# Optimization experiments

Measured on AMD Instinct MI355X. Metric: run time of the kernel, lower is better.

## Reference

```python
import jax, jax.numpy as jnp
import numpy as np

B, S, IN_DIM, H_DIM, OUT_DIM, N_LAYERS = 64, 1024, 256, 512, 256, 2


def setup_inputs() -> dict:
    key = jax.random.key(0)
    ks = jax.random.split(key, 16)
    scale = 0.05

    def W(k, shape):
        return (jax.random.normal(k, shape, jnp.float32) * scale)

    inp = {
        "input": jax.random.normal(ks[0], (B, S, IN_DIM), jnp.float32),
        "hidden_state": jnp.zeros((B, N_LAYERS, H_DIM), jnp.float32),
    }
    ki = 1
    for i in range(N_LAYERS):
        d_in = IN_DIM if i == 0 else H_DIM
        for g in ("z", "r", "g"):
            inp[f"W{g}_in_{i}"] = W(ks[ki], (d_in, H_DIM)); ki += 1
            inp[f"W{g}_h_{i}"] = W(ks[ki], (H_DIM, H_DIM)); ki += 1
            inp[f"b{g}_{i}"] = jnp.zeros((H_DIM,), jnp.float32)
    inp["Wo"] = W(ks[ki], (H_DIM, OUT_DIM)); ki += 1
    inp["bo"] = jnp.zeros((OUT_DIM,), jnp.float32)
    return inp


def _gru_layer(xs, h0, Wzi, Wzh, bz, Wri, Wrh, br, Wgi, Wgh, bg):
    # Precompute input projections for all timesteps (same math as per-step Linear).
    xz = jnp.einsum("bsi,ih->bsh", xs, Wzi)
    xr = jnp.einsum("bsi,ih->bsh", xs, Wri)
    xg = jnp.einsum("bsi,ih->bsh", xs, Wgi)

    def step(h, t):
        xz_t, xr_t, xg_t = t
        z = jax.nn.sigmoid(xz_t + h @ Wzh + bz)
        r = jax.nn.sigmoid(xr_t + h @ Wrh + br)
        g = jnp.tanh(xg_t + (h * r) @ Wgh + bg)
        h_new = z * h + (1.0 - z) * g
        return h_new, h_new

    h_last, hs = jax.lax.scan(
        step, h0,
        (jnp.swapaxes(xz, 0, 1), jnp.swapaxes(xr, 0, 1), jnp.swapaxes(xg, 0, 1)))
    return jnp.swapaxes(hs, 0, 1), h_last  # (B,S,H), (B,H)


def reference(input, hidden_state,
              Wz_in_0, Wz_h_0, bz_0, Wr_in_0, Wr_h_0, br_0, Wg_in_0, Wg_h_0, bg_0,
              Wz_in_1, Wz_h_1, bz_1, Wr_in_1, Wr_h_1, br_1, Wg_in_1, Wg_h_1, bg_1,
              Wo, bo):
    layers = [
        (Wz_in_0, Wz_h_0, bz_0, Wr_in_0, Wr_h_0, br_0, Wg_in_0, Wg_h_0, bg_0),
        (Wz_in_1, Wz_h_1, bz_1, Wr_in_1, Wr_h_1, br_1, Wg_in_1, Wg_h_1, bg_1),
    ]
    b = input.shape[0]
    seq = input
    finals = []
    for i, p in enumerate(layers):
        seq, h_last = _gru_layer(seq, hidden_state[:, i, :], *p)
        finals.append(h_last)
    y = jnp.einsum("bsh,ho->bso", seq, Wo) + bo
    # Faithful to original: torch.cat(layer_states) then reshape to (B, L, H)
    h_out = jnp.concatenate(finals, axis=0).reshape(b, len(layers), H_DIM)
    return y, h_out
```

## Files before the change

### kernel.cpp

```cpp
#include <hip/hip_runtime.h>
#include <stdint.h>

typedef unsigned short u16;
typedef short v8s __attribute__((ext_vector_type(8)));
typedef float v4f __attribute__((ext_vector_type(4)));

#define B_ 64
#define S_ 1024
#define IN_ 256
#define H_ 512
#define OUT_ 256
#define BS_ (B_ * S_)
#define GS_ ((size_t)BS_ * H_)
#define HP_ (H_ + 8)
#define KP1_ (1024 + 8)
#define FPAD_ 16

static __device__ __forceinline__ u16 f2bf(float f) {
  uint32_t u = __float_as_uint(f);
  u += 0x7FFFu + ((u >> 16) & 1u);
  return (u16)(u >> 16);
}
static __device__ __forceinline__ float bf2f(u16 h) {
  return __uint_as_float(((uint32_t)h) << 16);
}
static __device__ __forceinline__ v4f mfma16(v8s a, v8s b, v4f c) {
  return __builtin_amdgcn_mfma_f32_16x16x32_bf16(a, b, c, 0, 0, 0);
}
static __device__ __forceinline__ uint64_t cload64(const uint64_t* p) {
  return __hip_atomic_load(p, __ATOMIC_RELAXED, __HIP_MEMORY_SCOPE_AGENT);
}
static __device__ __forceinline__ void cstore64(uint64_t* p, uint64_t v) {
  __hip_atomic_store(p, v, __ATOMIC_RELAXED, __HIP_MEMORY_SCOPE_AGENT);
}
static __device__ __forceinline__ void cstore32(uint32_t* p, uint32_t v) {
  __hip_atomic_store(p, v, __ATOMIC_RELAXED, __HIP_MEMORY_SCOPE_AGENT);
}
static __device__ __forceinline__ void pollge(const uint32_t* p, uint32_t want) {
  while (__hip_atomic_load(p, __ATOMIC_RELAXED, __HIP_MEMORY_SCOPE_AGENT) < want)
    __builtin_amdgcn_s_sleep(1);
}
template <int NS>
static __device__ __forceinline__ void slab_barrier(uint32_t* flagbase,
                                                    int slab, uint32_t want,
                                                    int tid) {
  __syncthreads();
  if (tid == 0)
    __hip_atomic_store(flagbase + slab * FPAD_, want, __ATOMIC_RELAXED,
                       __HIP_MEMORY_SCOPE_AGENT);
  if (tid < NS) pollge(flagbase + tid * FPAD_, want);
  __syncthreads();
}

__global__ void cast_input_kernel(const float* __restrict__ src,
                                  u16* __restrict__ dst, int n4) {
  int i = blockIdx.x * blockDim.x + threadIdx.x;
  int stride = gridDim.x * blockDim.x;
  for (; i < n4; i += stride) {
    float4 v = ((const float4*)src)[i];
    uint32_t lo = (uint32_t)f2bf(v.x) | ((uint32_t)f2bf(v.y) << 16);
    uint32_t hi = (uint32_t)f2bf(v.z) | ((uint32_t)f2bf(v.w) << 16);
    ((uint2*)dst)[i] = make_uint2(lo, hi);
  }
}

__global__ void pack_transpose_k(const float* __restrict__ src,
                                 u16* __restrict__ dst, int K, int N,
                                 int dstK, int k0) {
  int i = blockIdx.x * blockDim.x + threadIdx.x;
  int total = K * N;
  int stride = gridDim.x * blockDim.x;
  for (; i < total; i += stride) {
    int n = i / K, k = i - n * K;
    dst[(size_t)n * dstK + k0 + k] = f2bf(src[(size_t)k * N + n]);
  }
}

__global__ void __launch_bounds__(256) gemm_kernel(
    const u16* __restrict__ A, const u16* __restrict__ Bt, int N, int K,
    u16* __restrict__ outb, float* __restrict__ outf,
    const float* __restrict__ bias, int mode) {
  const int bn = blockIdx.x * 64;
  const int bm = blockIdx.y * 64;
  const int w = threadIdx.x >> 6;
  const int lane = threadIdx.x & 63;
  const int wm = (w >> 1) * 32, wn = (w & 1) * 32;
  const int fr = lane & 15;
  const int kb = (lane >> 4) * 8;
  v4f acc00 = {0,0,0,0}, acc01 = {0,0,0,0}, acc10 = {0,0,0,0}, acc11 = {0,0,0,0};
  const u16* a0p = A + (size_t)(bm + wm + fr) * K + kb;
  const u16* a1p = a0p + (size_t)16 * K;
  const u16* b0p = Bt + (size_t)(bn + wn + fr) * K + kb;
  const u16* b1p = b0p + (size_t)16 * K;
  for (int kk = 0; kk < K; kk += 32) {
    v8s a0 = *(const v8s*)(a0p + kk);
    v8s a1 = *(const v8s*)(a1p + kk);
    v8s b0 = *(const v8s*)(b0p + kk);
    v8s b1 = *(const v8s*)(b1p + kk);
    acc00 = mfma16(a0, b0, acc00);
    acc01 = mfma16(a0, b1, acc01);
    acc10 = mfma16(a1, b0, acc10);
    acc11 = mfma16(a1, b1, acc11);
  }
  v4f accs[2][2] = {{acc00, acc01}, {acc10, acc11}};
  const int rb = (lane >> 4) * 4;
#pragma unroll
  for (int mi = 0; mi < 2; ++mi)
#pragma unroll
    for (int ni = 0; ni < 2; ++ni)
#pragma unroll
      for (int j = 0; j < 4; ++j) {
        int row = bm + wm + mi * 16 + rb + j;
        int col = bn + wn + ni * 16 + fr;
        float v = accs[mi][ni][j];
        if (mode == 0) {
          int gate = col >> 9, c = col & (H_ - 1);
          outb[(size_t)gate * GS_ + (size_t)row * H_ + c] = f2bf(v);
        } else {
          outf[(size_t)row * N + col] = v + bias[col];
        }
      }
}

__global__ void __launch_bounds__(256, 1) gru_pipe_kernel(
    const u16* xproj,
    const u16* __restrict__ Wht0,
    const u16* __restrict__ Wstk1,
    const float* __restrict__ bz0, const float* __restrict__ br0,
    const float* __restrict__ bg0,
    const float* __restrict__ bz1, const float* __restrict__ br1,
    const float* __restrict__ bg1,
    const float* __restrict__ hs,
    u16* h0buf,
    u16* hr0buf,
    u16* h1buf,
    u16* hr1buf,
    u16* seqout,
    float* __restrict__ hfinal,
    uint32_t* flags) {
  __shared__ __align__(16) char pool[134144];
  const int tid = threadIdx.x;
  const int bid = blockIdx.x;
  const int w = tid >> 6, lane = tid & 63;
  const int fr = lane & 15;
  const int kb = (lane >> 4) * 8;
  const int rb = (lane >> 4) * 4;

  if (bid < 64) {
    u16* ldsW = (u16*)pool;
    u16 (*ldsX)[HP_] = (u16(*)[HP_])(pool + 99840);
    float (*h32)[32] = (float(*)[32])(pool + 116480);
    const int grp = bid & 3;
    const int slab = bid >> 2;
    const int j0 = slab * 32;
    const int gb = grp * 16;

    for (int idx = tid; idx < 3 * 32 * 64; idx += 256) {
      int gate = idx >> 11;
      int rem = idx & 2047;
      int cl = rem >> 6;
      int kc = (rem & 63) * 8;
      *(v8s*)&ldsW[((gate * 32) + cl) * HP_ + kc] =
          *(const v8s*)(Wht0 + ((size_t)gate * H_ + (j0 + cl)) * H_ + kc);
    }
    for (int i = tid; i < 16 * H_; i += 256) {
      int row = i >> 9, col = i & (H_ - 1);
      ldsX[row][col] = f2bf(hs[((size_t)(gb + row) * 2 + 0) * H_ + col]);
    }
    for (int i = tid; i < 16 * 32; i += 256) {
      int row = i >> 5, cl = i & 31;
      h32[row][cl] = hs[((size_t)(gb + row) * 2 + 0) * H_ + j0 + cl];
    }
    __syncthreads();

    const int nt = w & 1;
    const int gateA = w >> 1;
    const int colL = nt * 16 + fr;
    const int gcol = j0 + colL;
    const float biasA = (gateA == 0) ? bz0[gcol] : br0[gcol];
    const float biasG = bg0[gcol];
    u16* hr0_g = hr0buf + (size_t)gb * H_;
    const u16* xA = xproj + (size_t)gateA * GS_;
    const u16* xG = xproj + (size_t)2 * GS_;
    const u16* wA = ldsW + ((size_t)(gateA * 32) + colL) * HP_;
    const u16* wG = ldsW + ((size_t)(2 * 32) + colL) * HP_;
    uint32_t* flagA0 = flags + (size_t)grp * 16 * FPAD_;
    uint32_t* flagB0 = flags + 1024 + (size_t)grp * 16 * FPAD_;
    uint32_t* c1g    = flags + 6144 + (size_t)grp * 32 * FPAD_;

    float zv0 = 0.f, zv1 = 0.f, zv2 = 0.f, zv3 = 0.f;

    for (int t = 0; t < S_; ++t) {
      if (t > 0) {
        if (t >= 2 && tid < 32) pollge(c1g + tid * FPAD_, (uint32_t)(t - 1));
        const uint64_t* src =
            (const uint64_t*)(h0buf + ((size_t)((t - 1) & 1) * B_ + gb) * H_);
        uint64_t vq[8];
#pragma unroll
        for (int i = 0; i < 8; ++i) vq[i] = cload64(src + i * 256 + tid);
#pragma unroll
        for (int i = 0; i < 8; ++i) {
          int d = i * 256 + tid;
          *(uint64_t*)&ldsX[d >> 7][(d & 127) * 4] = vq[i];
        }
        __syncthreads();
      }

      float xpre[4];
#pragma unroll
      for (int j = 0; j < 4; ++j)
        xpre[j] = bf2f(xA[((size_t)(gb + rb + j) * S_ + t) * H_ + gcol]);
      v4f acc0 = {0,0,0,0}, acc1 = {0,0,0,0};
#pragma unroll
      for (int kk = 0; kk < 8; ++kk) {
        acc0 = mfma16(*(const v8s*)&ldsX[fr][kk * 32 + kb],
                      *(const v8s*)(wA + kk * 32 + kb), acc0);
        acc1 = mfma16(*(const v8s*)&ldsX[fr][256 + kk * 32 + kb],
                      *(const v8s*)(wA + 256 + kk * 32 + kb), acc1);
      }
      float pre[4];
#pragma unroll
      for (int j = 0; j < 4; ++j) {
        float s = acc0[j] + acc1[j] + xpre[j] + biasA;
        pre[j] = 1.0f / (1.0f + __expf(-s));
      }
      if (gateA == 0) {
        zv0 = pre[0]; zv1 = pre[1]; zv2 = pre[2]; zv3 = pre[3];
      } else {
#pragma unroll
        for (int j = 0; j < 4; ++j) {
          float v = pre[j] * h32[rb + j][colL];
          float o1 = __shfl_xor(v, 1);
          uint32_t c0 = f2bf(v), c1 = f2bf(o1);
          uint32_t pk = (fr & 1) ? (c1 | (c0 << 16)) : (c0 | (c1 << 16));
          uint32_t pk2 = __shfl_xor(pk, 2);
          if ((fr & 3) == 0)
            cstore64((uint64_t*)&hr0_g[(size_t)(rb + j) * H_ + gcol],
                     (uint64_t)pk | ((uint64_t)pk2 << 32));
        }
      }
      asm volatile("s_waitcnt vmcnt(0)" ::: "memory");
      slab_barrier<16>(flagA0, slab, (uint32_t)(t + 1), tid);

      {
        const uint64_t* src = (const uint64_t*)hr0_g;
        uint64_t vq[8];
#pragma unroll
        for (int i = 0; i < 8; ++i) vq[i] = cload64(src + i * 256 + tid);
#pragma unroll
        for (int i = 0; i < 8; ++i) {
          int d = i * 256 + tid;
          *(uint64_t*)&ldsX[d >> 7][(d & 127) * 4] = vq[i];
        }
        __syncthreads();
      }

      if (w < 2) {
        float xpg[4];
#pragma unroll
        for (int j = 0; j < 4; ++j)
          xpg[j] = bf2f(xG[((size_t)(gb + rb + j) * S_ + t) * H_ + gcol]);
        v4f g0 = {0,0,0,0}, g1 = {0,0,0,0};
#pragma unroll
        for (int kk = 0; kk < 8; ++kk) {
          g0 = mfma16(*(const v8s*)&ldsX[fr][kk * 32 + kb],
                      *(const v8s*)(wG + kk * 32 + kb), g0);
          g1 = mfma16(*(const v8s*)&ldsX[fr][256 + kk * 32 + kb],
                      *(const v8s*)(wG + 256 + kk * 32 + kb), g1);
        }
        float zv[4] = {zv0, zv1, zv2, zv3};
        u16* h0dst = h0buf + ((size_t)(t & 1) * B_ + gb) * H_;
#pragma unroll
        for (int j = 0; j < 4; ++j) {
          int b = gb + rb + j;
          float gval = tanhf(g0[j] + g1[j] + xpg[j] + biasG);
          float hold = h32[rb + j][colL];
          float hnew = zv[j] * hold + (1.0f - zv[j]) * gval;
          h32[rb + j][colL] = hnew;
          uint32_t c0 = f2bf(hnew);
          float o1 = __shfl_xor(hnew, 1);
          uint32_t c1 = f2bf(o1);
          uint32_t pk = (fr & 1) ? (c1 | (c0 << 16)) : (c0 | (c1 << 16));
          uint32_t pk2 = __shfl_xor(pk, 2);
          if ((fr & 3) == 0)
            cstore64((uint64_t*)&h0dst[(size_t)(rb + j) * H_ + gcol],
                     (uint64_t)pk | ((uint64_t)pk2 << 32));
          if (t == S_ - 1) hfinal[(size_t)b * H_ + gcol] = hnew;
        }
      }
      asm volatile("s_waitcnt vmcnt(0)" ::: "memory");
      slab_barrier<16>(flagB0, slab, (uint32_t)(t + 1), tid);
    }
  } else {
    u16* ldsW = (u16*)pool;
    u16 (*ldsX)[KP1_] = (u16(*)[KP1_])(pool + 99072);
    float (*h32b)[16] = (float(*)[16])(pool + 132096);
    float (*xg32)[16] = (float(*)[16])(pool + 133120);
    const int b2 = bid - 64;
    const int grp = b2 & 3;
    const int slab = b2 >> 2;
    const int j0 = slab * 16;
    const int gb = grp * 16;
    const int gcol = j0 + fr;

    for (int idx = tid; idx < 3 * 16 * 128; idx += 256) {
      int gate = idx >> 11;
      int rem = idx & 2047;
      int cl = rem >> 7;
      int kc = (rem & 127) * 8;
      *(v8s*)&ldsW[((gate * 16) + cl) * KP1_ + kc] =
          *(const v8s*)(Wstk1 + ((size_t)(gate * H_) + (j0 + cl)) * 1024 + kc);
    }
    for (int i = tid; i < 16 * H_; i += 256) {
      int row = i >> 9, col = i & (H_ - 1);
      ldsX[row][512 + col] = f2bf(hs[((size_t)(gb + row) * 2 + 1) * H_ + col]);
    }
    for (int i = tid; i < 16 * 16; i += 256) {
      int row = i >> 4, c = i & 15;
      h32b[row][c] = hs[((size_t)(gb + row) * 2 + 1) * H_ + j0 + c];
    }
    __syncthreads();

    const float bzv = bz1[gcol], brv = br1[gcol], bgv = bg1[gcol];
    u16* h1_g = h1buf + (size_t)gb * H_;
    u16* hr1_g = hr1buf + (size_t)gb * H_;
    const u16* wZ = ldsW + ((size_t)(0 * 16) + fr) * KP1_;
    const u16* wR = ldsW + ((size_t)(1 * 16) + fr) * KP1_;
    const u16* wG = ldsW + ((size_t)(2 * 16) + fr) * KP1_;
    uint32_t* flagB0 = flags + 1024 + (size_t)grp * 16 * FPAD_;
    uint32_t* flagA1 = flags + 2048 + (size_t)grp * 32 * FPAD_;
    uint32_t* flagB1 = flags + 4096 + (size_t)grp * 32 * FPAD_;
    uint32_t* c1g    = flags + 6144 + (size_t)grp * 32 * FPAD_;
    float* hf1 = hfinal + (size_t)B_ * H_;

    float zv0 = 0.f, zv1 = 0.f, zv2 = 0.f, zv3 = 0.f;

    for (int t = 0; t < S_; ++t) {
      if (tid < 16) pollge(flagB0 + tid * FPAD_, (uint32_t)(t + 1));
      __syncthreads();
      {
        const uint64_t* s0 =
            (const uint64_t*)(h0buf + ((size_t)(t & 1) * B_ + gb) * H_);
        uint64_t q0[8];
#pragma unroll
        for (int i = 0; i < 8; ++i) q0[i] = cload64(s0 + i * 256 + tid);
        if (t > 0) {
          const uint64_t* s1 = (const uint64_t*)h1_g;
          uint64_t q1[8];
#pragma unroll
          for (int i = 0; i < 8; ++i) q1[i] = cload64(s1 + i * 256 + tid);
#pragma unroll
          for (int i = 0; i < 8; ++i) {
            int d = i * 256 + tid;
            *(uint64_t*)&ldsX[d >> 7][512 + (d & 127) * 4] = q1[i];
          }
        }
#pragma unroll
        for (int i = 0; i < 8; ++i) {
          int d = i * 256 + tid;
          *(uint64_t*)&ldsX[d >> 7][(d & 127) * 4] = q0[i];
        }
      }
      __syncthreads();
      if (tid == 0) cstore32(&c1g[slab * FPAD_], (uint32_t)(t + 1));

      if (w < 2) {
        const u16* wB = (w == 0) ? wZ : wR;
        v4f a0 = {0,0,0,0}, a1 = {0,0,0,0}, a2 = {0,0,0,0}, a3 = {0,0,0,0};
#pragma unroll
        for (int kk = 0; kk < 8; ++kk) {
          a0 = mfma16(*(const v8s*)&ldsX[fr][kk * 32 + kb],
                      *(const v8s*)(wB + kk * 32 + kb), a0);
          a1 = mfma16(*(const v8s*)&ldsX[fr][256 + kk * 32 + kb],
                      *(const v8s*)(wB + 256 + kk * 32 + kb), a1);
          a2 = mfma16(*(const v8s*)&ldsX[fr][512 + kk * 32 + kb],
                      *(const v8s*)(wB + 512 + kk * 32 + kb), a2);
          a3 = mfma16(*(const v8s*)&ldsX[fr][768 + kk * 32 + kb],
                      *(const v8s*)(wB + 768 + kk * 32 + kb), a3);
        }
        float pre[4];
#pragma unroll
        for (int j = 0; j < 4; ++j) {
          float s = a0[j] + a1[j] + a2[j] + a3[j] + ((w == 0) ? bzv : brv);
          pre[j] = 1.0f / (1.0f + __expf(-s));
        }
        if (w == 0) {
          zv0 = pre[0]; zv1 = pre[1]; zv2 = pre[2]; zv3 = pre[3];
        } else {
#pragma unroll
          for (int j = 0; j < 4; ++j) {
            float v = pre[j] * h32b[rb + j][fr];
            float o1 = __shfl_xor(v, 1);
            uint32_t c0 = f2bf(v), c1 = f2bf(o1);
            uint32_t pk = (fr & 1) ? (c1 | (c0 << 16)) : (c0 | (c1 << 16));
            uint32_t pk2 = __shfl_xor(pk, 2);
            if ((fr & 3) == 0)
              cstore64((uint64_t*)&hr1_g[(size_t)(rb + j) * H_ + gcol],
                       (uint64_t)pk | ((uint64_t)pk2 << 32));
          }
        }
      } else if (w == 2) {
        v4f a0 = {0,0,0,0}, a1 = {0,0,0,0};
#pragma unroll
        for (int kk = 0; kk < 8; ++kk) {
          a0 = mfma16(*(const v8s*)&ldsX[fr][kk * 32 + kb],
                      *(const v8s*)(wG + kk * 32 + kb), a0);
          a1 = mfma16(*(const v8s*)&ldsX[fr][256 + kk * 32 + kb],
                      *(const v8s*)(wG + 256 + kk * 32 + kb), a1);
        }
#pragma unroll
        for (int j = 0; j < 4; ++j) xg32[rb + j][fr] = a0[j] + a1[j];
      }
      asm volatile("s_waitcnt vmcnt(0)" ::: "memory");
      slab_barrier<32>(flagA1, slab, (uint32_t)(t + 1), tid);

      {
        const uint64_t* sr = (const uint64_t*)hr1_g;
        uint64_t q[8];
#pragma unroll
        for (int i = 0; i < 8; ++i) q[i] = cload64(sr + i * 256 + tid);
#pragma unroll
        for (int i = 0; i < 8; ++i) {
          int d = i * 256 + tid;
          *(uint64_t*)&ldsX[d >> 7][512 + (d & 127) * 4] = q[i];
        }
        __syncthreads();
      }

      if (w == 0) {
        v4f g0 = {0,0,0,0}, g1 = {0,0,0,0};
#pragma unroll
        for (int kk = 0; kk < 8; ++kk) {
          g0 = mfma16(*(const v8s*)&ldsX[fr][512 + kk * 32 + kb],
                      *(const v8s*)(wG + 512 + kk * 32 + kb), g0);
          g1 = mfma16(*(const v8s*)&ldsX[fr][768 + kk * 32 + kb],
                      *(const v8s*)(wG + 768 + kk * 32 + kb), g1);
        }
        float zv[4] = {zv0, zv1, zv2, zv3};
#pragma unroll
        for (int j = 0; j < 4; ++j) {
          int b = gb + rb + j;
          float gval = tanhf(g0[j] + g1[j] + xg32[rb + j][fr] + bgv);
          float hold = h32b[rb + j][fr];
          float hnew = zv[j] * hold + (1.0f - zv[j]) * gval;
          h32b[rb + j][fr] = hnew;
          uint32_t c0 = f2bf(hnew);
          float o1 = __shfl_xor(hnew, 1);
          uint32_t c1 = f2bf(o1);
          uint32_t pk = (fr & 1) ? (c1 | (c0 << 16)) : (c0 | (c1 << 16));
          uint32_t pk2 = __shfl_xor(pk, 2);
          if ((fr & 3) == 0) {
            uint64_t qv = (uint64_t)pk | ((uint64_t)pk2 << 32);
            cstore64((uint64_t*)&h1_g[(size_t)(rb + j) * H_ + gcol], qv);
            *(uint64_t*)&seqout[((size_t)b * S_ + t) * H_ + gcol] = qv;
          }
          if (t == S_ - 1) hf1[(size_t)b * H_ + gcol] = hnew;
        }
      }
      asm volatile("s_waitcnt vmcnt(0)" ::: "memory");
      slab_barrier<32>(flagB1, slab, (uint32_t)(t + 1), tid);
    }
  }
}

extern "C" void kernel_launch(void* const* d_in, const int* in_sizes, int n_in,
                              void* d_out, int out_size, void* d_ws,
                              size_t ws_size, hipStream_t stream) {
  const float* input = (const float*)d_in[0];
  const float* hs = (const float*)d_in[1];
  const float* W_in[2][3] = {
      {(const float*)d_in[2], (const float*)d_in[5], (const float*)d_in[8]},
      {(const float*)d_in[11], (const float*)d_in[14], (const float*)d_in[17]}};
  const float* W_h[2][3] = {
      {(const float*)d_in[3], (const float*)d_in[6], (const float*)d_in[9]},
      {(const float*)d_in[12], (const float*)d_in[15], (const float*)d_in[18]}};
  const float* bias[2][3] = {
      {(const float*)d_in[4], (const float*)d_in[7], (const float*)d_in[10]},
      {(const float*)d_in[13], (const float*)d_in[16], (const float*)d_in[19]}};
  const float* Wo = (const float*)d_in[20];
  const float* bo = (const float*)d_in[21];
  float* out = (float*)d_out;

  char* ws = (char*)d_ws;
  u16* xproj   = (u16*)(ws + 0);
  u16* wtin0   = (u16*)(ws + 201326592);
  u16* wth0    = (u16*)(ws + 202113024);
  u16* wstk1   = (u16*)(ws + 203685888);
  u16* wot     = (u16*)(ws + 206831616);
  u16* h0buf   = (u16*)(ws + 207093760);
  u16* hr0buf  = (u16*)(ws + 207224832);
  u16* h1buf   = (u16*)(ws + 207290368);
  u16* hr1buf  = (u16*)(ws + 207355904);
  uint32_t* flags = (uint32_t*)(ws + 207421440);

  u16* inbf = (u16*)d_out;
  u16* seq2 = xproj;

  cast_input_kernel<<<2048, 256, 0, stream>>>(input, inbf, BS_ * IN_ / 4);

  for (int g = 0; g < 3; ++g) {
    pack_transpose_k<<<256, 256, 0, stream>>>(
        W_in[0][g], wtin0 + (size_t)g * H_ * IN_, IN_, H_, IN_, 0);
    pack_transpose_k<<<256, 256, 0, stream>>>(
        W_h[0][g], wth0 + (size_t)g * H_ * H_, H_, H_, H_, 0);
    pack_transpose_k<<<256, 256, 0, stream>>>(
        W_in[1][g], wstk1 + (size_t)g * H_ * 1024, H_, H_, 1024, 0);
    pack_transpose_k<<<256, 256, 0, stream>>>(
        W_h[1][g], wstk1 + (size_t)g * H_ * 1024, H_, H_, 1024, 512);
  }
  pack_transpose_k<<<256, 256, 0, stream>>>(Wo, wot, H_, OUT_, H_, 0);

  gemm_kernel<<<dim3(24, 1024), 256, 0, stream>>>(
      inbf, wtin0, 1536, IN_, xproj, nullptr, nullptr, 0);

  hipMemsetAsync(flags, 0, 32768, stream);
  const size_t ysz = (size_t)BS_ * OUT_;
  float* hfin = out + ysz;
  gru_pipe_kernel<<<dim3(192), dim3(256), 0, stream>>>(
      xproj, wth0, wstk1, bias[0][0], bias[0][1], bias[0][2], bias[1][0],
      bias[1][1], bias[1][2], hs, h0buf, hr0buf, h1buf, hr1buf, seq2, hfin,
      flags);

  gemm_kernel<<<dim3(4, 1024), 256, 0, stream>>>(seq2, wot, OUT_, H_, nullptr,
                                                 out, bo, 1);
}
```

Baseline: 7.386 ms.

## Replace slab flag barriers with per-element tagged data words in GRU exchange

Each bf16 hidden value is now stored in a 32-bit word together with a 16-bit timestep tag, so consumers check the data itself for freshness instead of waiting on separate per-slab flag barriers and vmcnt drains. This removes the store-drain and flag-poll round trips around each exchange of h and h*r between workgroups; consumers spot-poll tail words and then re-poll individual words while staging into LDS. The cost is twice the exchange buffer traffic, larger unrolled staging loops and a larger memset, and the tag wraps at 65536, which is safe for 1024 steps. The x-projection load for the candidate gate is also hoisted ahead of the first matmul.

```diff
diff --git a/kernel.cpp b/kernel.cpp
--- a/kernel.cpp
+++ b/kernel.cpp
@@ -15,6 +15,7 @@
 #define HP_ (H_ + 8)
 #define KP1_ (1024 + 8)
 #define FPAD_ 16
+#define TMASK_ 0x0000FFFF0000FFFFull
 
 static __device__ __forceinline__ u16 f2bf(float f) {
   uint32_t u = __float_as_uint(f);
@@ -40,16 +41,57 @@
   while (__hip_atomic_load(p, __ATOMIC_RELAXED, __HIP_MEMORY_SCOPE_AGENT) < want)
     __builtin_amdgcn_s_sleep(1);
 }
-template <int NS>
-static __device__ __forceinline__ void slab_barrier(uint32_t* flagbase,
-                                                    int slab, uint32_t want,
-                                                    int tid) {
-  __syncthreads();
-  if (tid == 0)
-    __hip_atomic_store(flagbase + slab * FPAD_, want, __ATOMIC_RELAXED,
-                       __HIP_MEMORY_SCOPE_AGENT);
-  if (tid < NS) pollge(flagbase + tid * FPAD_, want);
-  __syncthreads();
+static __device__ __forceinline__ uint64_t tagpat(uint32_t tag) {
+  return (uint64_t)tag * 0x0000000100000001ull;
+}
+static __device__ __forceinline__ void polltag(const uint64_t* p, uint64_t pat) {
+  while ((cload64(p) ^ pat) & TMASK_) __builtin_amdgcn_s_sleep(1);
+}
+static __device__ __forceinline__ void store_pair(uint32_t* blk, int row,
+                                                  int gcol, float v, int fr,
+                                                  uint32_t tag) {
+  float o1 = __shfl_xor(v, 1);
+  if ((fr & 1) == 0) {
+    uint64_t qv = (uint64_t)(((uint32_t)f2bf(v) << 16) | tag) |
+                  ((uint64_t)(((uint32_t)f2bf(o1) << 16) | tag) << 32);
+    cstore64((uint64_t*)(blk + (size_t)row * 512 + gcol), qv);
+  }
+}
+static __device__ __forceinline__ void stage2(const uint64_t* a64, uint64_t pa,
+                                              u16* la, const uint64_t* b64,
+                                              uint64_t pb, u16* lb, int rs,
+                                              int tid) {
+  uint64_t qa[16], qb[16];
+#pragma unroll
+  for (int i = 0; i < 16; ++i) qa[i] = cload64(a64 + i * 256 + tid);
+  if (b64) {
+#pragma unroll
+    for (int i = 0; i < 16; ++i) qb[i] = cload64(b64 + i * 256 + tid);
+  }
+#pragma unroll
+  for (int i = 0; i < 16; ++i) {
+    while ((qa[i] ^ pa) & TMASK_) {
+      __builtin_amdgcn_s_sleep(1);
+      qa[i] = cload64(a64 + i * 256 + tid);
+    }
+    int d = i * 256 + tid;
+    *(uint32_t*)(la + (size_t)(d >> 8) * rs + (d & 255) * 2) =
+        ((uint32_t)(qa[i] >> 16) & 0xFFFFu) |
+        ((uint32_t)(qa[i] >> 32) & 0xFFFF0000u);
+  }
+  if (b64) {
+#pragma unroll
+    for (int i = 0; i < 16; ++i) {
+      while ((qb[i] ^ pb) & TMASK_) {
+        __builtin_amdgcn_s_sleep(1);
+        qb[i] = cload64(b64 + i * 256 + tid);
+      }
+      int d = i * 256 + tid;
+      *(uint32_t*)(lb + (size_t)(d >> 8) * rs + (d & 255) * 2) =
+          ((uint32_t)(qb[i] >> 16) & 0xFFFFu) |
+          ((uint32_t)(qb[i] >> 32) & 0xFFFF0000u);
+    }
+  }
 }
 
 __global__ void cast_input_kernel(const float* __restrict__ src,
@@ -131,13 +173,13 @@
     const float* __restrict__ bz1, const float* __restrict__ br1,
     const float* __restrict__ bg1,
     const float* __restrict__ hs,
-    u16* h0buf,
-    u16* hr0buf,
-    u16* h1buf,
-    u16* hr1buf,
+    uint32_t* h0x,
+    uint32_t* hr0x,
+    uint32_t* h1x,
+    uint32_t* hr1x,
     u16* seqout,
     float* __restrict__ hfinal,
-    uint32_t* flags) {
+    uint32_t* c1g) {
   __shared__ __align__(16) char pool[134144];
   const int tid = threadIdx.x;
   const int bid = blockIdx.x;
@@ -179,37 +221,39 @@
     const int gcol = j0 + colL;
     const float biasA = (gateA == 0) ? bz0[gcol] : br0[gcol];
     const float biasG = bg0[gcol];
-    u16* hr0_g = hr0buf + (size_t)gb * H_;
+    uint32_t* hr0b = hr0x + (size_t)grp * 8192;
+    uint32_t* c1gg = c1g + (size_t)grp * 32 * FPAD_;
     const u16* xA = xproj + (size_t)gateA * GS_;
     const u16* xG = xproj + (size_t)2 * GS_;
     const u16* wA = ldsW + ((size_t)(gateA * 32) + colL) * HP_;
     const u16* wG = ldsW + ((size_t)(2 * 32) + colL) * HP_;
-    uint32_t* flagA0 = flags + (size_t)grp * 16 * FPAD_;
-    uint32_t* flagB0 = flags + 1024 + (size_t)grp * 16 * FPAD_;
-    uint32_t* c1g    = flags + 6144 + (size_t)grp * 32 * FPAD_;
-
-    float zv0 = 0.f, zv1 = 0.f, zv2 = 0.f, zv3 = 0.f;
+
+    float zv[4] = {0.f, 0.f, 0.f, 0.f};
 
     for (int t = 0; t < S_; ++t) {
       if (t > 0) {
-        if (t >= 2 && tid < 32) pollge(c1g + tid * FPAD_, (uint32_t)(t - 1));
-        const uint64_t* src =
-            (const uint64_t*)(h0buf + ((size_t)((t - 1) & 1) * B_ + gb) * H_);
-        uint64_t vq[8];
-#pragma unroll
-        for (int i = 0; i < 8; ++i) vq[i] = cload64(src + i * 256 + tid);
-#pragma unroll
-        for (int i = 0; i < 8; ++i) {
-          int d = i * 256 + tid;
-          *(uint64_t*)&ldsX[d >> 7][(d & 127) * 4] = vq[i];
-        }
+        const uint64_t* b64 =
+            (const uint64_t*)(h0x + (size_t)(((t - 1) & 1) * 4 + grp) * 8192);
+        if (t >= 2 && tid < 32) pollge(c1gg + tid * FPAD_, (uint32_t)(t - 1));
+        if (tid < 16) polltag(b64 + 3840 + 16 * tid, tagpat((uint32_t)t));
         __syncthreads();
-      }
-
-      float xpre[4];
-#pragma unroll
-      for (int j = 0; j < 4; ++j)
-        xpre[j] = bf2f(xA[((size_t)(gb + rb + j) * S_ + t) * H_ + gcol]);
+        stage2(b64, tagpat((uint32_t)t), &ldsX[0][0], nullptr, 0, nullptr,
+               HP_, tid);
+        __syncthreads();
+      }
+
+      float xpre[4], xpg[4];
+      if (w < 2) {
+#pragma unroll
+        for (int j = 0; j < 4; ++j) {
+          xpre[j] = bf2f(xA[((size_t)(gb + rb + j) * S_ + t) * H_ + gcol]);
+          xpg[j] = bf2f(xG[((size_t)(gb + rb + j) * S_ + t) * H_ + gcol]);
+        }
+      } else {
+#pragma unroll
+        for (int j = 0; j < 4; ++j)
+          xpre[j] = bf2f(xA[((size_t)(gb + rb + j) * S_ + t) * H_ + gcol]);
+      }
       v4f acc0 = {0,0,0,0}, acc1 = {0,0,0,0};
 #pragma unroll
       for (int kk = 0; kk < 8; ++kk) {
@@ -225,41 +269,24 @@
         pre[j] = 1.0f / (1.0f + __expf(-s));
       }
       if (gateA == 0) {
-        zv0 = pre[0]; zv1 = pre[1]; zv2 = pre[2]; zv3 = pre[3];
+#pragma unroll
+        for (int j = 0; j < 4; ++j) zv[j] = pre[j];
       } else {
 #pragma unroll
         for (int j = 0; j < 4; ++j) {
           float v = pre[j] * h32[rb + j][colL];
-          float o1 = __shfl_xor(v, 1);
-          uint32_t c0 = f2bf(v), c1 = f2bf(o1);
-          uint32_t pk = (fr & 1) ? (c1 | (c0 << 16)) : (c0 | (c1 << 16));
-          uint32_t pk2 = __shfl_xor(pk, 2);
-          if ((fr & 3) == 0)
-            cstore64((uint64_t*)&hr0_g[(size_t)(rb + j) * H_ + gcol],
-                     (uint64_t)pk | ((uint64_t)pk2 << 32));
-        }
-      }
-      asm volatile("s_waitcnt vmcnt(0)" ::: "memory");
-      slab_barrier<16>(flagA0, slab, (uint32_t)(t + 1), tid);
-
-      {
-        const uint64_t* src = (const uint64_t*)hr0_g;
-        uint64_t vq[8];
-#pragma unroll
-        for (int i = 0; i < 8; ++i) vq[i] = cload64(src + i * 256 + tid);
-#pragma unroll
-        for (int i = 0; i < 8; ++i) {
-          int d = i * 256 + tid;
-          *(uint64_t*)&ldsX[d >> 7][(d & 127) * 4] = vq[i];
-        }
-        __syncthreads();
-      }
+          store_pair(hr0b, rb + j, gcol, v, fr, (uint32_t)(t + 1));
+        }
+      }
+      if (tid < 16)
+        polltag((const uint64_t*)hr0b + 3840 + 16 * tid,
+                tagpat((uint32_t)(t + 1)));
+      __syncthreads();
+      stage2((const uint64_t*)hr0b, tagpat((uint32_t)(t + 1)), &ldsX[0][0],
+             nullptr, 0, nullptr, HP_, tid);
+      __syncthreads();
 
       if (w < 2) {
-        float xpg[4];
-#pragma unroll
-        for (int j = 0; j < 4; ++j)
-          xpg[j] = bf2f(xG[((size_t)(gb + rb + j) * S_ + t) * H_ + gcol]);
         v4f g0 = {0,0,0,0}, g1 = {0,0,0,0};
 #pragma unroll
         for (int kk = 0; kk < 8; ++kk) {
@@ -268,8 +295,7 @@
           g1 = mfma16(*(const v8s*)&ldsX[fr][256 + kk * 32 + kb],
                       *(const v8s*)(wG + 256 + kk * 32 + kb), g1);
         }
-        float zv[4] = {zv0, zv1, zv2, zv3};
-        u16* h0dst = h0buf + ((size_t)(t & 1) * B_ + gb) * H_;
+        uint32_t* h0slot = h0x + (size_t)((t & 1) * 4 + grp) * 8192;
 #pragma unroll
         for (int j = 0; j < 4; ++j) {
           int b = gb + rb + j;
@@ -277,19 +303,10 @@
           float hold = h32[rb + j][colL];
           float hnew = zv[j] * hold + (1.0f - zv[j]) * gval;
           h32[rb + j][colL] = hnew;
-          uint32_t c0 = f2bf(hnew);
-          float o1 = __shfl_xor(hnew, 1);
-          uint32_t c1 = f2bf(o1);
-          uint32_t pk = (fr & 1) ? (c1 | (c0 << 16)) : (c0 | (c1 << 16));
-          uint32_t pk2 = __shfl_xor(pk, 2);
-          if ((fr & 3) == 0)
-            cstore64((uint64_t*)&h0dst[(size_t)(rb + j) * H_ + gcol],
-                     (uint64_t)pk | ((uint64_t)pk2 << 32));
+          store_pair(h0slot, rb + j, gcol, hnew, fr, (uint32_t)(t + 1));
           if (t == S_ - 1) hfinal[(size_t)b * H_ + gcol] = hnew;
         }
       }
-      asm volatile("s_waitcnt vmcnt(0)" ::: "memory");
-      slab_barrier<16>(flagB0, slab, (uint32_t)(t + 1), tid);
     }
   } else {
     u16* ldsW = (u16*)pool;
@@ -322,47 +339,29 @@
     __syncthreads();
 
     const float bzv = bz1[gcol], brv = br1[gcol], bgv = bg1[gcol];
-    u16* h1_g = h1buf + (size_t)gb * H_;
-    u16* hr1_g = hr1buf + (size_t)gb * H_;
+    uint32_t* h1b = h1x + (size_t)grp * 8192;
+    uint32_t* hr1b = hr1x + (size_t)grp * 8192;
+    uint32_t* c1gg = c1g + (size_t)grp * 32 * FPAD_;
     const u16* wZ = ldsW + ((size_t)(0 * 16) + fr) * KP1_;
     const u16* wR = ldsW + ((size_t)(1 * 16) + fr) * KP1_;
     const u16* wG = ldsW + ((size_t)(2 * 16) + fr) * KP1_;
-    uint32_t* flagB0 = flags + 1024 + (size_t)grp * 16 * FPAD_;
-    uint32_t* flagA1 = flags + 2048 + (size_t)grp * 32 * FPAD_;
-    uint32_t* flagB1 = flags + 4096 + (size_t)grp * 32 * FPAD_;
-    uint32_t* c1g    = flags + 6144 + (size_t)grp * 32 * FPAD_;
     float* hf1 = hfinal + (size_t)B_ * H_;
 
-    float zv0 = 0.f, zv1 = 0.f, zv2 = 0.f, zv3 = 0.f;
+    float zv[4] = {0.f, 0.f, 0.f, 0.f};
 
     for (int t = 0; t < S_; ++t) {
-      if (tid < 16) pollge(flagB0 + tid * FPAD_, (uint32_t)(t + 1));
+      const uint64_t* b064 =
+          (const uint64_t*)(h0x + (size_t)((t & 1) * 4 + grp) * 8192);
+      if (tid < 16) polltag(b064 + 3840 + 16 * tid, tagpat((uint32_t)(t + 1)));
+      else if (t > 0 && tid < 48)
+        polltag((const uint64_t*)h1b + 3840 + 8 * (tid - 16),
+                tagpat((uint32_t)t));
       __syncthreads();
-      {
-        const uint64_t* s0 =
-            (const uint64_t*)(h0buf + ((size_t)(t & 1) * B_ + gb) * H_);
-        uint64_t q0[8];
-#pragma unroll
-        for (int i = 0; i < 8; ++i) q0[i] = cload64(s0 + i * 256 + tid);
-        if (t > 0) {
-          const uint64_t* s1 = (const uint64_t*)h1_g;
-          uint64_t q1[8];
-#pragma unroll
-          for (int i = 0; i < 8; ++i) q1[i] = cload64(s1 + i * 256 + tid);
-#pragma unroll
-          for (int i = 0; i < 8; ++i) {
-            int d = i * 256 + tid;
-            *(uint64_t*)&ldsX[d >> 7][512 + (d & 127) * 4] = q1[i];
-          }
-        }
-#pragma unroll
-        for (int i = 0; i < 8; ++i) {
-          int d = i * 256 + tid;
-          *(uint64_t*)&ldsX[d >> 7][(d & 127) * 4] = q0[i];
-        }
-      }
+      stage2(b064, tagpat((uint32_t)(t + 1)), &ldsX[0][0],
+             (t > 0) ? (const uint64_t*)h1b : nullptr, tagpat((uint32_t)t),
+             &ldsX[0][512], KP1_, tid);
       __syncthreads();
-      if (tid == 0) cstore32(&c1g[slab * FPAD_], (uint32_t)(t + 1));
+      if (tid == 0) cstore32(&c1gg[slab * FPAD_], (uint32_t)(t + 1));
 
       if (w < 2) {
         const u16* wB = (w == 0) ? wZ : wR;
@@ -385,18 +384,13 @@
           pre[j] = 1.0f / (1.0f + __expf(-s));
         }
         if (w == 0) {
-          zv0 = pre[0]; zv1 = pre[1]; zv2 = pre[2]; zv3 = pre[3];
+#pragma unroll
+          for (int j = 0; j < 4; ++j) zv[j] = pre[j];
         } else {
 #pragma unroll
           for (int j = 0; j < 4; ++j) {
             float v = pre[j] * h32b[rb + j][fr];
-            float o1 = __shfl_xor(v, 1);
-            uint32_t c0 = f2bf(v), c1 = f2bf(o1);
-            uint32_t pk = (fr & 1) ? (c1 | (c0 << 16)) : (c0 | (c1 << 16));
-            uint32_t pk2 = __shfl_xor(pk, 2);
-            if ((fr & 3) == 0)
-              cstore64((uint64_t*)&hr1_g[(size_t)(rb + j) * H_ + gcol],
-                       (uint64_t)pk | ((uint64_t)pk2 << 32));
+            store_pair(hr1b, rb + j, gcol, v, fr, (uint32_t)(t + 1));
           }
         }
       } else if (w == 2) {
@@ -411,21 +405,13 @@
 #pragma unroll
         for (int j = 0; j < 4; ++j) xg32[rb + j][fr] = a0[j] + a1[j];
       }
-      asm volatile("s_waitcnt vmcnt(0)" ::: "memory");
-      slab_barrier<32>(flagA1, slab, (uint32_t)(t + 1), tid);
-
-      {
-        const uint64_t* sr = (const uint64_t*)hr1_g;
-        uint64_t q[8];
-#pragma unroll
-        for (int i = 0; i < 8; ++i) q[i] = cload64(sr + i * 256 + tid);
-#pragma unroll
-        for (int i = 0; i < 8; ++i) {
-          int d = i * 256 + tid;
-          *(uint64_t*)&ldsX[d >> 7][512 + (d & 127) * 4] = q[i];
-        }
-        __syncthreads();
-      }
+      if (tid < 32)
+        polltag((const uint64_t*)hr1b + 3840 + 8 * tid,
+                tagpat((uint32_t)(t + 1)));
+      __syncthreads();
+      stage2((const uint64_t*)hr1b, tagpat((uint32_t)(t + 1)), &ldsX[0][512],
+             nullptr, 0, nullptr, KP1_, tid);
+      __syncthreads();
 
       if (w == 0) {
         v4f g0 = {0,0,0,0}, g1 = {0,0,0,0};
@@ -436,7 +422,6 @@
           g1 = mfma16(*(const v8s*)&ldsX[fr][768 + kk * 32 + kb],
                       *(const v8s*)(wG + 768 + kk * 32 + kb), g1);
         }
-        float zv[4] = {zv0, zv1, zv2, zv3};
 #pragma unroll
         for (int j = 0; j < 4; ++j) {
           int b = gb + rb + j;
@@ -444,6 +429,7 @@
           float hold = h32b[rb + j][fr];
           float hnew = zv[j] * hold + (1.0f - zv[j]) * gval;
           h32b[rb + j][fr] = hnew;
+          store_pair(h1b, rb + j, gcol, hnew, fr, (uint32_t)(t + 1));
           uint32_t c0 = f2bf(hnew);
           float o1 = __shfl_xor(hnew, 1);
           uint32_t c1 = f2bf(o1);
@@ -451,14 +437,11 @@
           uint32_t pk2 = __shfl_xor(pk, 2);
           if ((fr & 3) == 0) {
             uint64_t qv = (uint64_t)pk | ((uint64_t)pk2 << 32);
-            cstore64((uint64_t*)&h1_g[(size_t)(rb + j) * H_ + gcol], qv);
             *(uint64_t*)&seqout[((size_t)b * S_ + t) * H_ + gcol] = qv;
           }
           if (t == S_ - 1) hf1[(size_t)b * H_ + gcol] = hnew;
         }
       }
-      asm volatile("s_waitcnt vmcnt(0)" ::: "memory");
-      slab_barrier<32>(flagB1, slab, (uint32_t)(t + 1), tid);
     }
   }
 }
@@ -487,11 +470,11 @@
   u16* wth0    = (u16*)(ws + 202113024);
   u16* wstk1   = (u16*)(ws + 203685888);
   u16* wot     = (u16*)(ws + 206831616);
-  u16* h0buf   = (u16*)(ws + 207093760);
-  u16* hr0buf  = (u16*)(ws + 207224832);
-  u16* h1buf   = (u16*)(ws + 207290368);
-  u16* hr1buf  = (u16*)(ws + 207355904);
-  uint32_t* flags = (uint32_t*)(ws + 207421440);
+  uint32_t* h0x  = (uint32_t*)(ws + 207093760);
+  uint32_t* hr0x = (uint32_t*)(ws + 207355904);
+  uint32_t* h1x  = (uint32_t*)(ws + 207486976);
+  uint32_t* hr1x = (uint32_t*)(ws + 207618048);
+  uint32_t* c1g  = (uint32_t*)(ws + 207749120);
 
   u16* inbf = (u16*)d_out;
   u16* seq2 = xproj;
@@ -513,13 +496,12 @@
   gemm_kernel<<<dim3(24, 1024), 256, 0, stream>>>(
       inbf, wtin0, 1536, IN_, xproj, nullptr, nullptr, 0);
 
-  hipMemsetAsync(flags, 0, 32768, stream);
+  hipMemsetAsync(h0x, 0, 663552, stream);
   const size_t ysz = (size_t)BS_ * OUT_;
   float* hfin = out + ysz;
   gru_pipe_kernel<<<dim3(192), dim3(256), 0, stream>>>(
       xproj, wth0, wstk1, bias[0][0], bias[0][1], bias[0][2], bias[1][0],
-      bias[1][1], bias[1][2], hs, h0buf, hr0buf, h1buf, hr1buf, seq2, hfin,
-      flags);
+      bias[1][1], bias[1][2], hs, h0x, hr0x, h1x, hr1x, seq2, hfin, c1g);
 
   gemm_kernel<<<dim3(4, 1024), 256, 0, stream>>>(seq2, wot, OUT_, H_, nullptr,
                                                  out, bo, 1);
```

Measured after the change: 8.050 ms. +9.0%, slower.

## Replace end-of-step slab barriers with deferred flag waits and quad-buffered h0

Applied to the files above, without the earlier changes.

The end-of-step barrier in both layer-0 and layer-1 blocks becomes a non-blocking flag publish. The wait moves to the start of the next step and is merged with the cross-layer consumer flag check, both polled by one wavefront. The h0 buffer grows from double to quadruple buffering, so layer 0 can run up to three steps ahead of layer 1. Input-projection loads are hoisted to the top of the step to overlap with the wait, and layer 1 writes its sequence output after publishing its flag. This shortens the serial critical path per timestep, at the cost of more workspace and subtler cross-block ordering.

```diff
diff --git a/kernel.cpp b/kernel.cpp
--- a/kernel.cpp
+++ b/kernel.cpp
@@ -36,9 +36,8 @@
 static __device__ __forceinline__ void cstore32(uint32_t* p, uint32_t v) {
   __hip_atomic_store(p, v, __ATOMIC_RELAXED, __HIP_MEMORY_SCOPE_AGENT);
 }
-static __device__ __forceinline__ void pollge(const uint32_t* p, uint32_t want) {
-  while (__hip_atomic_load(p, __ATOMIC_RELAXED, __HIP_MEMORY_SCOPE_AGENT) < want)
-    __builtin_amdgcn_s_sleep(1);
+static __device__ __forceinline__ uint32_t cload32(const uint32_t* p) {
+  return __hip_atomic_load(p, __ATOMIC_RELAXED, __HIP_MEMORY_SCOPE_AGENT);
 }
 template <int NS>
 static __device__ __forceinline__ void slab_barrier(uint32_t* flagbase,
@@ -48,8 +47,18 @@
   if (tid == 0)
     __hip_atomic_store(flagbase + slab * FPAD_, want, __ATOMIC_RELAXED,
                        __HIP_MEMORY_SCOPE_AGENT);
-  if (tid < NS) pollge(flagbase + tid * FPAD_, want);
+  if (tid < NS) {
+    while (cload32(flagbase + tid * FPAD_) < want) __builtin_amdgcn_s_sleep(1);
+  }
   __syncthreads();
+}
+static __device__ __forceinline__ void pack_store4(u16* dst, float v, int fr) {
+  float o1 = __shfl_xor(v, 1);
+  uint32_t c0 = f2bf(v), c1 = f2bf(o1);
+  uint32_t pk = (fr & 1) ? (c1 | (c0 << 16)) : (c0 | (c1 << 16));
+  uint32_t pk2 = __shfl_xor(pk, 2);
+  if ((fr & 3) == 0)
+    cstore64((uint64_t*)dst, (uint64_t)pk | ((uint64_t)pk2 << 32));
 }
 
 __global__ void cast_input_kernel(const float* __restrict__ src,
@@ -186,15 +195,33 @@
     const u16* wG = ldsW + ((size_t)(2 * 32) + colL) * HP_;
     uint32_t* flagA0 = flags + (size_t)grp * 16 * FPAD_;
     uint32_t* flagB0 = flags + 1024 + (size_t)grp * 16 * FPAD_;
-    uint32_t* c1g    = flags + 6144 + (size_t)grp * 32 * FPAD_;
-
-    float zv0 = 0.f, zv1 = 0.f, zv2 = 0.f, zv3 = 0.f;
+    uint32_t* c1gg   = flags + 6144 + (size_t)grp * 32 * FPAD_;
+
+    float zv[4] = {0.f, 0.f, 0.f, 0.f};
 
     for (int t = 0; t < S_; ++t) {
+      u16 xa_[4], xg_[4];
+#pragma unroll
+      for (int j = 0; j < 4; ++j) {
+        size_t off = ((size_t)(gb + rb + j) * S_ + t) * H_ + gcol;
+        xa_[j] = xA[off];
+        if (w < 2) xg_[j] = xG[off];
+      }
+
       if (t > 0) {
-        if (t >= 2 && tid < 32) pollge(c1g + tid * FPAD_, (uint32_t)(t - 1));
+        if (w == 0) {
+          const uint32_t* pa = flagB0;
+          uint32_t want = 0;
+          if (lane < 16) { pa = flagB0 + lane * FPAD_; want = (uint32_t)t; }
+          else if (lane < 48) {
+            pa = c1gg + (lane - 16) * FPAD_;
+            if (t >= 4) want = (uint32_t)(t - 3);
+          }
+          while (cload32(pa) < want) __builtin_amdgcn_s_sleep(1);
+        }
+        __syncthreads();
         const uint64_t* src =
-            (const uint64_t*)(h0buf + ((size_t)((t - 1) & 1) * B_ + gb) * H_);
+            (const uint64_t*)(h0buf + ((size_t)((t - 1) & 3) * B_ + gb) * H_);
         uint64_t vq[8];
 #pragma unroll
         for (int i = 0; i < 8; ++i) vq[i] = cload64(src + i * 256 + tid);
@@ -206,10 +233,6 @@
         __syncthreads();
       }
 
-      float xpre[4];
-#pragma unroll
-      for (int j = 0; j < 4; ++j)
-        xpre[j] = bf2f(xA[((size_t)(gb + rb + j) * S_ + t) * H_ + gcol]);
       v4f acc0 = {0,0,0,0}, acc1 = {0,0,0,0};
 #pragma unroll
       for (int kk = 0; kk < 8; ++kk) {
@@ -221,23 +244,17 @@
       float pre[4];
 #pragma unroll
       for (int j = 0; j < 4; ++j) {
-        float s = acc0[j] + acc1[j] + xpre[j] + biasA;
+        float s = acc0[j] + acc1[j] + bf2f(xa_[j]) + biasA;
         pre[j] = 1.0f / (1.0f + __expf(-s));
       }
       if (gateA == 0) {
-        zv0 = pre[0]; zv1 = pre[1]; zv2 = pre[2]; zv3 = pre[3];
+#pragma unroll
+        for (int j = 0; j < 4; ++j) zv[j] = pre[j];
       } else {
 #pragma unroll
-        for (int j = 0; j < 4; ++j) {
-          float v = pre[j] * h32[rb + j][colL];
-          float o1 = __shfl_xor(v, 1);
-          uint32_t c0 = f2bf(v), c1 = f2bf(o1);
-          uint32_t pk = (fr & 1) ? (c1 | (c0 << 16)) : (c0 | (c1 << 16));
-          uint32_t pk2 = __shfl_xor(pk, 2);
-          if ((fr & 3) == 0)
-            cstore64((uint64_t*)&hr0_g[(size_t)(rb + j) * H_ + gcol],
-                     (uint64_t)pk | ((uint64_t)pk2 << 32));
-        }
+        for (int j = 0; j < 4; ++j)
+          pack_store4(&hr0_g[(size_t)(rb + j) * H_ + gcol],
+                      pre[j] * h32[rb + j][colL], fr);
       }
       asm volatile("s_waitcnt vmcnt(0)" ::: "memory");
       slab_barrier<16>(flagA0, slab, (uint32_t)(t + 1), tid);
@@ -256,10 +273,6 @@
       }
 
       if (w < 2) {
-        float xpg[4];
-#pragma unroll
-        for (int j = 0; j < 4; ++j)
-          xpg[j] = bf2f(xG[((size_t)(gb + rb + j) * S_ + t) * H_ + gcol]);
         v4f g0 = {0,0,0,0}, g1 = {0,0,0,0};
 #pragma unroll
         for (int kk = 0; kk < 8; ++kk) {
@@ -268,28 +281,22 @@
           g1 = mfma16(*(const v8s*)&ldsX[fr][256 + kk * 32 + kb],
                       *(const v8s*)(wG + 256 + kk * 32 + kb), g1);
         }
-        float zv[4] = {zv0, zv1, zv2, zv3};
-        u16* h0dst = h0buf + ((size_t)(t & 1) * B_ + gb) * H_;
+        u16* h0dst = h0buf + ((size_t)(t & 3) * B_ + gb) * H_;
 #pragma unroll
         for (int j = 0; j < 4; ++j) {
           int b = gb + rb + j;
-          float gval = tanhf(g0[j] + g1[j] + xpg[j] + biasG);
+          float gval = tanhf(g0[j] + g1[j] + bf2f(xg_[j]) + biasG);
           float hold = h32[rb + j][colL];
           float hnew = zv[j] * hold + (1.0f - zv[j]) * gval;
           h32[rb + j][colL] = hnew;
-          uint32_t c0 = f2bf(hnew);
-          float o1 = __shfl_xor(hnew, 1);
-          uint32_t c1 = f2bf(o1);
-          uint32_t pk = (fr & 1) ? (c1 | (c0 << 16)) : (c0 | (c1 << 16));
-          uint32_t pk2 = __shfl_xor(pk, 2);
-          if ((fr & 3) == 0)
-            cstore64((uint64_t*)&h0dst[(size_t)(rb + j) * H_ + gcol],
-                     (uint64_t)pk | ((uint64_t)pk2 << 32));
+          pack_store4(&h0dst[(size_t)(rb + j) * H_ + gcol], hnew, fr);
           if (t == S_ - 1) hfinal[(size_t)b * H_ + gcol] = hnew;
         }
       }
       asm volatile("s_waitcnt vmcnt(0)" ::: "memory");
-      slab_barrier<16>(flagB0, slab, (uint32_t)(t + 1), tid);
+      __syncthreads();
+      if (tid == 0)
+        cstore32(flagB0 + slab * FPAD_, (uint32_t)(t + 1));
     }
   } else {
     u16* ldsW = (u16*)pool;
@@ -330,17 +337,26 @@
     uint32_t* flagB0 = flags + 1024 + (size_t)grp * 16 * FPAD_;
     uint32_t* flagA1 = flags + 2048 + (size_t)grp * 32 * FPAD_;
     uint32_t* flagB1 = flags + 4096 + (size_t)grp * 32 * FPAD_;
-    uint32_t* c1g    = flags + 6144 + (size_t)grp * 32 * FPAD_;
+    uint32_t* c1gg   = flags + 6144 + (size_t)grp * 32 * FPAD_;
     float* hf1 = hfinal + (size_t)B_ * H_;
 
-    float zv0 = 0.f, zv1 = 0.f, zv2 = 0.f, zv3 = 0.f;
+    float zv[4] = {0.f, 0.f, 0.f, 0.f};
 
     for (int t = 0; t < S_; ++t) {
-      if (tid < 16) pollge(flagB0 + tid * FPAD_, (uint32_t)(t + 1));
+      if (w == 0) {
+        const uint32_t* pa = flagB0;
+        uint32_t want = 0;
+        if (lane < 16) { pa = flagB0 + lane * FPAD_; want = (uint32_t)(t + 1); }
+        else if (lane < 48) {
+          pa = flagB1 + (lane - 16) * FPAD_;
+          want = (uint32_t)t;
+        }
+        while (cload32(pa) < want) __builtin_amdgcn_s_sleep(1);
+      }
       __syncthreads();
       {
         const uint64_t* s0 =
-            (const uint64_t*)(h0buf + ((size_t)(t & 1) * B_ + gb) * H_);
+            (const uint64_t*)(h0buf + ((size_t)((t & 3)) * B_ + gb) * H_);
         uint64_t q0[8];
 #pragma unroll
         for (int i = 0; i < 8; ++i) q0[i] = cload64(s0 + i * 256 + tid);
@@ -362,7 +378,7 @@
         }
       }
       __syncthreads();
-      if (tid == 0) cstore32(&c1g[slab * FPAD_], (uint32_t)(t + 1));
+      if (tid == 0) cstore32(&c1gg[slab * FPAD_], (uint32_t)(t + 1));
 
       if (w < 2) {
         const u16* wB = (w == 0) ? wZ : wR;
@@ -385,19 +401,13 @@
           pre[j] = 1.0f / (1.0f + __expf(-s));
         }
         if (w == 0) {
-          zv0 = pre[0]; zv1 = pre[1]; zv2 = pre[2]; zv3 = pre[3];
+#pragma unroll
+          for (int j = 0; j < 4; ++j) zv[j] = pre[j];
         } else {
 #pragma unroll
-          for (int j = 0; j < 4; ++j) {
-            float v = pre[j] * h32b[rb + j][fr];
-            float o1 = __shfl_xor(v, 1);
-            uint32_t c0 = f2bf(v), c1 = f2bf(o1);
-            uint32_t pk = (fr & 1) ? (c1 | (c0 << 16)) : (c0 | (c1 << 16));
-            uint32_t pk2 = __shfl_xor(pk, 2);
-            if ((fr & 3) == 0)
-              cstore64((uint64_t*)&hr1_g[(size_t)(rb + j) * H_ + gcol],
-                       (uint64_t)pk | ((uint64_t)pk2 << 32));
-          }
+          for (int j = 0; j < 4; ++j)
+            pack_store4(&hr1_g[(size_t)(rb + j) * H_ + gcol],
+                        pre[j] * h32b[rb + j][fr], fr);
         }
       } else if (w == 2) {
         v4f a0 = {0,0,0,0}, a1 = {0,0,0,0};
@@ -427,6 +437,8 @@
         __syncthreads();
       }
 
+      uint64_t qsv[4];
+      float hn[4];
       if (w == 0) {
         v4f g0 = {0,0,0,0}, g1 = {0,0,0,0};
 #pragma unroll
@@ -436,29 +448,36 @@
           g1 = mfma16(*(const v8s*)&ldsX[fr][768 + kk * 32 + kb],
                       *(const v8s*)(wG + 768 + kk * 32 + kb), g1);
         }
-        float zv[4] = {zv0, zv1, zv2, zv3};
 #pragma unroll
         for (int j = 0; j < 4; ++j) {
-          int b = gb + rb + j;
           float gval = tanhf(g0[j] + g1[j] + xg32[rb + j][fr] + bgv);
           float hold = h32b[rb + j][fr];
           float hnew = zv[j] * hold + (1.0f - zv[j]) * gval;
           h32b[rb + j][fr] = hnew;
-          uint32_t c0 = f2bf(hnew);
+          hn[j] = hnew;
           float o1 = __shfl_xor(hnew, 1);
-          uint32_t c1 = f2bf(o1);
+          uint32_t c0 = f2bf(hnew), c1 = f2bf(o1);
           uint32_t pk = (fr & 1) ? (c1 | (c0 << 16)) : (c0 | (c1 << 16));
           uint32_t pk2 = __shfl_xor(pk, 2);
-          if ((fr & 3) == 0) {
-            uint64_t qv = (uint64_t)pk | ((uint64_t)pk2 << 32);
+          uint64_t qv = (uint64_t)pk | ((uint64_t)pk2 << 32);
+          qsv[j] = qv;
+          if ((fr & 3) == 0)
             cstore64((uint64_t*)&h1_g[(size_t)(rb + j) * H_ + gcol], qv);
-            *(uint64_t*)&seqout[((size_t)b * S_ + t) * H_ + gcol] = qv;
-          }
-          if (t == S_ - 1) hf1[(size_t)b * H_ + gcol] = hnew;
         }
       }
       asm volatile("s_waitcnt vmcnt(0)" ::: "memory");
-      slab_barrier<32>(flagB1, slab, (uint32_t)(t + 1), tid);
+      __syncthreads();
+      if (tid == 0) cstore32(flagB1 + slab * FPAD_, (uint32_t)(t + 1));
+
+      if (w == 0) {
+#pragma unroll
+        for (int j = 0; j < 4; ++j) {
+          int b = gb + rb + j;
+          if ((fr & 3) == 0)
+            *(uint64_t*)&seqout[((size_t)b * S_ + t) * H_ + gcol] = qsv[j];
+          if (t == S_ - 1) hf1[(size_t)b * H_ + gcol] = hn[j];
+        }
+      }
     }
   }
 }
@@ -488,10 +507,10 @@
   u16* wstk1   = (u16*)(ws + 203685888);
   u16* wot     = (u16*)(ws + 206831616);
   u16* h0buf   = (u16*)(ws + 207093760);
-  u16* hr0buf  = (u16*)(ws + 207224832);
-  u16* h1buf   = (u16*)(ws + 207290368);
-  u16* hr1buf  = (u16*)(ws + 207355904);
-  uint32_t* flags = (uint32_t*)(ws + 207421440);
+  u16* hr0buf  = (u16*)(ws + 207355904);
+  u16* h1buf   = (u16*)(ws + 207421440);
+  u16* hr1buf  = (u16*)(ws + 207486976);
+  uint32_t* flags = (uint32_t*)(ws + 207552512);
 
   u16* inbf = (u16*)d_out;
   u16* seq2 = xproj;
```

Result: faster. 6.686 ms (-9.5%).
